# Kernel tuning notes

Measured on AMD Instinct MI355X. Metric: run time of the kernel, lower is better.

## Reference

```python
import jax, jax.numpy as jnp
import numpy as np

B, L1, L2, D, H, V, C = 32, 512, 16, 300, 300, 50000, 3


def setup_inputs() -> dict:
    key = jax.random.key(0)
    ks = jax.random.split(key, 20)
    s_emb = 1.0 / np.sqrt(D)
    s_h = 1.0 / np.sqrt(H)
    inp = {
        "context_ids": jax.random.randint(ks[0], (B, L1), 0, V),
        "aspect_ids": jax.random.randint(ks[1], (B, L2), 0, V),
        "context_masks": jnp.ones((B, L1), dtype=bool),
        "aspect_masks": jnp.ones((B, L2), dtype=bool),
        # frozen pretrained embedding table
        "emb": jax.random.normal(ks[2], (V, D), jnp.float32) * 0.1,
        # Attention module (no biases)
        "Wc": jax.random.normal(ks[3], (D, D), jnp.float32) * s_emb,
        "Wa": jax.random.normal(ks[4], (D, D), jnp.float32) * s_emb,
        "Vatt": jax.random.normal(ks[5], (1, D), jnp.float32) * s_emb,
        # self.W / self.V linears
        "Wlin": jax.random.normal(ks[6], (D, D), jnp.float32) * s_emb,
        "blin": jnp.zeros((D,), jnp.float32),
        "Vw": jax.random.normal(ks[7], (1, D), jnp.float32) * s_emb,
        "bVw": jnp.zeros((1,), jnp.float32),
        # bidirectional GRU, PyTorch layout: weight_ih (3H, D), weight_hh (3H, H)
        "wih_f": jax.random.normal(ks[8], (3 * H, D), jnp.float32) * s_h,
        "whh_f": jax.random.normal(ks[9], (3 * H, H), jnp.float32) * s_h,
        "bih_f": jnp.zeros((3 * H,), jnp.float32),
        "bhh_f": jnp.zeros((3 * H,), jnp.float32),
        "wih_b": jax.random.normal(ks[10], (3 * H, D), jnp.float32) * s_h,
        "whh_b": jax.random.normal(ks[11], (3 * H, H), jnp.float32) * s_h,
        "bih_b": jnp.zeros((3 * H,), jnp.float32),
        "bhh_b": jnp.zeros((3 * H,), jnp.float32),
        # output projection over concat(fwd, bwd) hidden
        "outW": jax.random.normal(ks[12], (C, 2 * H), jnp.float32) * (1.0 / np.sqrt(2 * H)),
        "outb": jnp.zeros((C,), jnp.float32),
    }
    return inp


def _gru_dir(x, wih, whh, bih, bhh, reverse):
    # x: (B, T, D) -> (B, T, H). PyTorch gate order: r, z, n.
    xg = jnp.einsum('btd,gd->btg', x, wih) + bih          # (B, T, 3H)
    xg = jnp.swapaxes(xg, 0, 1)                            # (T, B, 3H)

    def step(h, xg_t):
        rx, zx, nx = jnp.split(xg_t, 3, axis=-1)
        hg = h @ whh.T + bhh
        rh, zh, nh = jnp.split(hg, 3, axis=-1)
        r = jax.nn.sigmoid(rx + rh)
        z = jax.nn.sigmoid(zx + zh)
        n = jnp.tanh(nx + r * nh)
        h_new = (1.0 - z) * n + z * h
        return h_new, h_new

    h0 = jnp.zeros((x.shape[0], whh.shape[1]), x.dtype)
    _, hs = jax.lax.scan(step, h0, xg, reverse=reverse)
    return jnp.swapaxes(hs, 0, 1)                          # (B, T, H)


def reference(context_ids, aspect_ids, context_masks, aspect_masks, emb,
              Wc, Wa, Vatt, Wlin, blin, Vw, bVw,
              wih_f, whh_f, bih_f, bhh_f, wih_b, whh_b, bih_b, bhh_b,
              outW, outb):
    context = emb[context_ids]                             # (B, L1, D)
    aspect = emb[aspect_ids]                               # (B, L2, D)

    # additive (Bahdanau) attention: broadcast tanh score over (L1, L2)
    c = jnp.einsum('bld,ed->ble', context, Wc)             # (B, L1, D)
    a = jnp.einsum('bmd,ed->bme', aspect, Wa)              # (B, L2, D)
    s = jnp.tanh(c[:, :, None, :] + a[:, None, :, :])      # (B, L1, L2, D)
    scores = jnp.einsum('blmd,d->blm', s, Vatt[0])         # (B, L1, L2)
    alpha = jax.nn.softmax(scores, axis=-1)                # softmax over L2
    context_ = jnp.einsum('blm,bmd->bld', alpha, aspect)   # (B, L1, D)

    aaaa = jnp.tanh(jnp.einsum('bld,ed->ble', context, Wlin) + blin + context_)
    beta = jax.nn.softmax(jnp.einsum('bld,od->blo', aaaa, Vw) + bVw, axis=1)  # (B, L1, 1)

    h_f = _gru_dir(context, wih_f, whh_f, bih_f, bhh_f, reverse=False)
    h_b = _gru_dir(context, wih_b, whh_b, bih_b, bhh_b, reverse=True)
    senti_seq = jnp.concatenate([h_f, h_b], axis=-1)       # (B, L1, 2H)

    senti = jnp.einsum('bl,blh->bh', beta[..., 0], senti_seq)  # (B, 2H)
    logit = senti @ outW.T + outb                          # (B, C)
    return logit
```

## Files before the change

### kernel.cpp

```cpp
#include <hip/hip_runtime.h>

#define B_  32
#define L1_ 512
#define L2_ 16
#define D_  300
#define H_  300

__device__ __forceinline__ float sigmoid_fast(float x) {
    return 1.0f / (1.0f + __expf(-x));
}
__device__ __forceinline__ float tanh_fast(float x) {
    x = fminf(fmaxf(x, -15.0f), 15.0f);
    float e = __expf(2.0f * x);
    return (e - 1.0f) / (e + 1.0f);
}
__device__ __forceinline__ float sigmoid_acc(float x) {
    return 1.0f / (1.0f + expf(-x));
}
__device__ __forceinline__ float wred_sum(float v) {
    #pragma unroll
    for (int off = 32; off > 0; off >>= 1) v += __shfl_xor(v, off);
    return v;
}
__device__ __forceinline__ float wred_max(float v) {
    #pragma unroll
    for (int off = 32; off > 0; off >>= 1) v = fmaxf(v, __shfl_xor(v, off));
    return v;
}

__device__ __forceinline__ void store_pkt(long long* p, long long v) {
    asm volatile("global_store_dwordx2 %0, %1, off sc0 sc1" :: "v"(p), "v"(v) : "memory");
}
__device__ __forceinline__ long long load_pkt(const long long* p) {
    long long v;
    asm volatile("global_load_dwordx2 %0, %1, off sc0 sc1\n\t"
                 "s_waitcnt vmcnt(0)"
                 : "=v"(v) : "v"(p) : "memory");
    return v;
}

__global__ __launch_bounds__(256) void gather_kernel(const float* __restrict__ emb,
                                                     const int* __restrict__ ids,
                                                     float* __restrict__ out, int total) {
    for (int i = blockIdx.x * 256 + threadIdx.x; i < total; i += gridDim.x * 256) {
        int row = i / 75, c = i % 75;
        int id = ids[row];
        reinterpret_cast<float4*>(out)[i] =
            reinterpret_cast<const float4*>(emb + (size_t)id * 300)[c];
    }
}

#define TM 128
#define TN 64
#define TK 16
__global__ __launch_bounds__(256) void gemm_nt(const float* __restrict__ A,
                                               const float* __restrict__ W,
                                               const float* __restrict__ bias,
                                               float* __restrict__ C,
                                               int M, int N, int K) {
    __shared__ __align__(16) float As[TK][TM + 4];
    __shared__ __align__(16) float Bs[TK][TN + 4];
    const int tid = threadIdx.x;
    const int m0 = blockIdx.x * TM;
    const int n0 = blockIdx.y * TN;
    const int tx = tid & 15;
    const int ty = tid >> 4;
    const int lr = tid >> 2;
    const int lk = (tid & 3) << 2;

    float acc[8][4];
    #pragma unroll
    for (int i = 0; i < 8; ++i)
        #pragma unroll
        for (int j = 0; j < 4; ++j) acc[i][j] = 0.f;

    for (int k0 = 0; k0 < K; k0 += TK) {
        const bool kok = (k0 + lk + 3) < K;
        #pragma unroll
        for (int h = 0; h < 2; ++h) {
            float4 v = make_float4(0.f, 0.f, 0.f, 0.f);
            int m = m0 + lr + 64 * h;
            if (kok) v = *reinterpret_cast<const float4*>(&A[(size_t)m * K + k0 + lk]);
            As[lk + 0][lr + 64 * h] = v.x;
            As[lk + 1][lr + 64 * h] = v.y;
            As[lk + 2][lr + 64 * h] = v.z;
            As[lk + 3][lr + 64 * h] = v.w;
        }
        {
            float4 v = make_float4(0.f, 0.f, 0.f, 0.f);
            int n = n0 + lr;
            if (kok && n < N) v = *reinterpret_cast<const float4*>(&W[(size_t)n * K + k0 + lk]);
            Bs[lk + 0][lr] = v.x;
            Bs[lk + 1][lr] = v.y;
            Bs[lk + 2][lr] = v.z;
            Bs[lk + 3][lr] = v.w;
        }
        __syncthreads();
        #pragma unroll
        for (int k = 0; k < TK; ++k) {
            float4 a0 = *reinterpret_cast<const float4*>(&As[k][ty * 8]);
            float4 a1 = *reinterpret_cast<const float4*>(&As[k][ty * 8 + 4]);
            float4 bv = *reinterpret_cast<const float4*>(&Bs[k][tx * 4]);
            float av[8] = {a0.x, a0.y, a0.z, a0.w, a1.x, a1.y, a1.z, a1.w};
            float bb[4] = {bv.x, bv.y, bv.z, bv.w};
            #pragma unroll
            for (int i = 0; i < 8; ++i)
                #pragma unroll
                for (int j = 0; j < 4; ++j) acc[i][j] += av[i] * bb[j];
        }
        __syncthreads();
    }
    #pragma unroll
    for (int i = 0; i < 8; ++i) {
        int m = m0 + ty * 8 + i;
        #pragma unroll
        for (int j = 0; j < 4; ++j) {
            int n = n0 + tx * 4 + j;
            if (n < N) C[(size_t)m * N + n] = acc[i][j] + (bias ? bias[n] : 0.f);
        }
    }
}

__global__ __launch_bounds__(256) void attn_kernel(const float* __restrict__ c_proj,
                                                   const float* __restrict__ a_proj,
                                                   const float* __restrict__ asp_emb,
                                                   const float* __restrict__ lin,
                                                   const float* __restrict__ Vatt,
                                                   const float* __restrict__ Vw,
                                                   const float* __restrict__ bVw,
                                                   float* __restrict__ blogit) {
    const int b = blockIdx.y;
    const int chunk = blockIdx.x;
    __shared__ float sA[16 * 300];
    __shared__ float sE[16 * 300];
    __shared__ float sV[300];
    __shared__ float sW[300];
    const int tid = threadIdx.x;
    for (int i = tid; i < 16 * 300; i += 256) {
        sA[i] = a_proj[b * 4800 + i];
        sE[i] = asp_emb[b * 4800 + i];
    }
    for (int i = tid; i < 300; i += 256) {
        sV[i] = Vatt[i];
        sW[i] = Vw[i];
    }
    __syncthreads();
    const int wave = tid >> 6, lane = tid & 63;
    const float bvw = bVw[0];
    for (int li = 0; li < 4; ++li) {
        const int l = chunk * 16 + wave * 4 + li;
        const float* crow = c_proj + (size_t)(b * L1_ + l) * 300;
        float cr[5];
        #pragma unroll
        for (int i = 0; i < 5; ++i) {
            int d = lane + 64 * i;
            cr[i] = (d < 300) ? crow[d] : 0.f;
        }
        float sc[16];
        #pragma unroll
        for (int m = 0; m < 16; ++m) {
            float s = 0.f;
            #pragma unroll
            for (int i = 0; i < 5; ++i) {
                int d = lane + 64 * i;
                if (d < 300) s += tanh_fast(cr[i] + sA[m * 300 + d]) * sV[d];
            }
            s = wred_sum(s);
            sc[m] = s;
        }
        float mx = sc[0];
        #pragma unroll
        for (int m = 1; m < 16; ++m) mx = fmaxf(mx, sc[m]);
        float den = 0.f;
        #pragma unroll
        for (int m = 0; m < 16; ++m) {
            sc[m] = __expf(sc[m] - mx);
            den += sc[m];
        }
        const float inv = 1.f / den;
        const float* lrow = lin + (size_t)(b * L1_ + l) * 300;
        float acc = 0.f;
        #pragma unroll
        for (int i = 0; i < 5; ++i) {
            int d = lane + 64 * i;
            if (d < 300) {
                float cd = 0.f;
                #pragma unroll
                for (int m = 0; m < 16; ++m) cd += sc[m] * sE[m * 300 + d];
                acc += tanh_fast(lrow[d] + cd * inv) * sW[d];
            }
        }
        acc = wred_sum(acc);
        if (lane == 0) blogit[b * L1_ + l] = acc + bvw;
    }
}

__global__ __launch_bounds__(256) void beta_softmax_kernel(const float* __restrict__ x,
                                                           float* __restrict__ y) {
    const int b = blockIdx.x, tid = threadIdx.x;
    __shared__ float red[4];
    const int wave = tid >> 6, lane = tid & 63;
    float v0 = x[b * 512 + tid];
    float v1 = x[b * 512 + 256 + tid];
    float m = wred_max(fmaxf(v0, v1));
    if (lane == 0) red[wave] = m;
    __syncthreads();
    m = fmaxf(fmaxf(red[0], red[1]), fmaxf(red[2], red[3]));
    float e0 = __expf(v0 - m), e1 = __expf(v1 - m);
    float s = wred_sum(e0 + e1);
    __syncthreads();
    if (lane == 0) red[wave] = s;
    __syncthreads();
    s = red[0] + red[1] + red[2] + red[3];
    const float inv = 1.f / s;
    y[b * 512 + tid] = e0 * inv;
    y[b * 512 + 256 + tid] = e1 * inv;
}

__global__ __launch_bounds__(256, 1) void gru7_kernel(const float* __restrict__ xg_f,
                                                      const float* __restrict__ xg_b,
                                                      const float* __restrict__ whh_f,
                                                      const float* __restrict__ whh_b,
                                                      const float* __restrict__ bhh_f,
                                                      const float* __restrict__ bhh_b,
                                                      const float* __restrict__ beta,
                                                      long long* __restrict__ slot,
                                                      float* __restrict__ senti) {
    const int s = blockIdx.x;
    const int b = blockIdx.y;
    const int rev = blockIdx.z;
    const int g = rev * 32 + b;
    const float* xg  = rev ? xg_b : xg_f;
    const float* whh = rev ? whh_b : whh_f;
    const float* bhh = rev ? bhh_b : bhh_f;

    const int tid = threadIdx.x;
    const int e0 = s * 75;
    const bool act = tid < 225;
    const int gate = tid / 75;
    const int idx = tid % 75;

    __shared__ __align__(16) float hs[304];
    __shared__ float gg[3][80];

    float4 w4[75];
    float bh = 0.f;
    if (act) {
        const int row = gate * 300 + e0 + idx;
        bh = bhh[row];
        const float4* wp = reinterpret_cast<const float4*>(whh + (size_t)row * 300);
        #pragma unroll
        for (int j = 0; j < 75; ++j) w4[j] = wp[j];
    } else {
        #pragma unroll
        for (int j = 0; j < 75; ++j) w4[j] = make_float4(0.f, 0.f, 0.f, 0.f);
    }
    #pragma unroll
    for (int j = 0; j < 75; ++j)
        asm volatile("" : "+v"(w4[j].x), "+v"(w4[j].y), "+v"(w4[j].z), "+v"(w4[j].w));
    asm volatile("" : "+v"(bh));

    int fsl = 0, fli = 0;
    const long long* rp0 = nullptr;
    if (tid < 225) {
        fsl = tid / 75;
        if (fsl >= s) ++fsl;
        fli = tid % 75;
    }
    long long* wp0 = slot + ((size_t)g * 4 + s) * 80 + tid;
    const long long* rbase = slot + ((size_t)g * 4 + fsl) * 80 + fli;

    for (int i = tid; i < 304; i += 256) hs[i] = 0.f;
    float sacc = 0.f;
    int gaveup = 0;
    __syncthreads();

    const float4* hs4 = reinterpret_cast<const float4*>(hs);
    for (int step = 0; step < 512; ++step) {
        const int t = rev ? (511 - step) : step;
        float xr = 0.f, xz = 0.f, xn = 0.f, bt = 0.f;
        if (tid < 75) {
            const float* xrow = xg + (size_t)(b * 512 + t) * 900;
            const int e = e0 + tid;
            xr = xrow[e];
            xz = xrow[300 + e];
            xn = xrow[600 + e];
            bt = beta[b * 512 + t];
        }
        float a0 = 0.f, a1 = 0.f, a2 = 0.f, a3 = 0.f;
        #pragma unroll
        for (int j = 0; j < 72; j += 4) {
            float4 hv;
            hv = hs4[j];
            a0 = fmaf(w4[j].x, hv.x, a0); a0 = fmaf(w4[j].y, hv.y, a0);
            a0 = fmaf(w4[j].z, hv.z, a0); a0 = fmaf(w4[j].w, hv.w, a0);
            hv = hs4[j + 1];
            a1 = fmaf(w4[j + 1].x, hv.x, a1); a1 = fmaf(w4[j + 1].y, hv.y, a1);
            a1 = fmaf(w4[j + 1].z, hv.z, a1); a1 = fmaf(w4[j + 1].w, hv.w, a1);
            hv = hs4[j + 2];
            a2 = fmaf(w4[j + 2].x, hv.x, a2); a2 = fmaf(w4[j + 2].y, hv.y, a2);
            a2 = fmaf(w4[j + 2].z, hv.z, a2); a2 = fmaf(w4[j + 2].w, hv.w, a2);
            hv = hs4[j + 3];
            a3 = fmaf(w4[j + 3].x, hv.x, a3); a3 = fmaf(w4[j + 3].y, hv.y, a3);
            a3 = fmaf(w4[j + 3].z, hv.z, a3); a3 = fmaf(w4[j + 3].w, hv.w, a3);
        }
        {
            float4 hv;
            hv = hs4[72];
            a0 = fmaf(w4[72].x, hv.x, a0); a0 = fmaf(w4[72].y, hv.y, a0);
            a0 = fmaf(w4[72].z, hv.z, a0); a0 = fmaf(w4[72].w, hv.w, a0);
            hv = hs4[73];
            a1 = fmaf(w4[73].x, hv.x, a1); a1 = fmaf(w4[73].y, hv.y, a1);
            a1 = fmaf(w4[73].z, hv.z, a1); a1 = fmaf(w4[73].w, hv.w, a1);
            hv = hs4[74];
            a2 = fmaf(w4[74].x, hv.x, a2); a2 = fmaf(w4[74].y, hv.y, a2);
            a2 = fmaf(w4[74].z, hv.z, a2); a2 = fmaf(w4[74].w, hv.w, a2);
        }
        const float acc = bh + ((a0 + a1) + (a2 + a3));
        if (act) gg[gate][idx] = acc;
        __syncthreads();
        if (tid < 75) {
            const int e = e0 + tid;
            const float rr = sigmoid_acc(xr + gg[0][tid]);
            const float zz = sigmoid_acc(xz + gg[1][tid]);
            const float nn = tanhf(xn + rr * gg[2][tid]);
            const float hn = (1.f - zz) * nn + zz * hs[e];
            sacc = fmaf(bt, hn, sacc);
            hs[e] = hn;
            if (step < 511) {
                long long pkt = ((long long)(unsigned)step << 32) |
                                (unsigned)__float_as_int(hn);
                store_pkt(wp0 + (size_t)(step & 1) * 64 * 4 * 80, pkt);
            }
        }
        if (step == 511) break;
        if (tid < 225) {
            const long long* p = rbase + (size_t)(step & 1) * 64 * 4 * 80;
            long long v = 0;
            if (!gaveup) {
                int ok = 0;
                for (int it = 0; it < (1 << 16); ++it) {
                    v = load_pkt(p);
                    if (((int)(v >> 32)) == step) { ok = 1; break; }
                }
                if (!ok) gaveup = 1;
            } else {
                v = load_pkt(p);
            }
            hs[fsl * 75 + fli] = __int_as_float((int)(v & 0xffffffffLL));
        }
        __syncthreads();
    }
    if (tid < 75) senti[b * 600 + rev * 300 + e0 + tid] = sacc;
}

__global__ __launch_bounds__(64) void logits_kernel(const float* __restrict__ senti,
                                                    const float* __restrict__ outW,
                                                    const float* __restrict__ outb,
                                                    float* __restrict__ out) {
    const int b = blockIdx.x, lane = threadIdx.x;
    for (int c = 0; c < 3; ++c) {
        float s = 0.f;
        for (int hh = lane; hh < 600; hh += 64) s += senti[b * 600 + hh] * outW[c * 600 + hh];
        s = wred_sum(s);
        if (lane == 0) out[b * 3 + c] = s + outb[c];
    }
}

extern "C" void kernel_launch(void* const* d_in, const int* in_sizes, int n_in,
                              void* d_out, int out_size, void* d_ws, size_t ws_size,
                              hipStream_t stream) {
    const int* ctx_ids = (const int*)d_in[0];
    const int* asp_ids = (const int*)d_in[1];
    const float* emb   = (const float*)d_in[4];
    const float* Wc    = (const float*)d_in[5];
    const float* Wa    = (const float*)d_in[6];
    const float* Vatt  = (const float*)d_in[7];
    const float* Wlin  = (const float*)d_in[8];
    const float* blin  = (const float*)d_in[9];
    const float* Vw    = (const float*)d_in[10];
    const float* bVw   = (const float*)d_in[11];
    const float* wih_f = (const float*)d_in[12];
    const float* whh_f = (const float*)d_in[13];
    const float* bih_f = (const float*)d_in[14];
    const float* bhh_f = (const float*)d_in[15];
    const float* wih_b = (const float*)d_in[16];
    const float* whh_b = (const float*)d_in[17];
    const float* bih_b = (const float*)d_in[18];
    const float* bhh_b = (const float*)d_in[19];
    const float* outW  = (const float*)d_in[20];
    const float* outb  = (const float*)d_in[21];
    float* ws = (float*)d_ws;

    size_t o = 0;
    float* ctx_emb = ws + o; o += (size_t)B_ * L1_ * D_;
    float* asp_emb = ws + o; o += (size_t)B_ * L2_ * D_;
    float* c_proj  = ws + o; o += (size_t)B_ * L1_ * D_;
    float* a_proj  = ws + o; o += (size_t)B_ * L2_ * D_;
    float* lin_buf = ws + o; o += (size_t)B_ * L1_ * D_;
    float* xg_f    = ws + o; o += (size_t)B_ * L1_ * 3 * H_;
    float* xg_b    = ws + o; o += (size_t)B_ * L1_ * 3 * H_;
    float* blogit  = ws + o; o += (size_t)B_ * L1_;
    float* beta    = ws + o; o += (size_t)B_ * L1_;
    float* senti   = ws + o; o += (size_t)B_ * 2 * H_;
    o = (o + 1) & ~(size_t)1;
    long long* slot = (long long*)(ws + o);
    const size_t slot_ll = (size_t)2 * 64 * 4 * 80;
    o += slot_ll * 2;

    hipMemsetAsync(slot, 0xFF, slot_ll * sizeof(long long), stream);

    dim3 blk(256);
    const int tot_ctx = B_ * L1_ * 75;
    const int tot_asp = B_ * L2_ * 75;
    gather_kernel<<<dim3((tot_ctx + 255) / 256), blk, 0, stream>>>(emb, ctx_ids, ctx_emb, tot_ctx);
    gather_kernel<<<dim3((tot_asp + 255) / 256), blk, 0, stream>>>(emb, asp_ids, asp_emb, tot_asp);

    gemm_nt<<<dim3(16384 / 128, 5), blk, 0, stream>>>(ctx_emb, Wc, nullptr, c_proj, 16384, 300, 300);
    gemm_nt<<<dim3(16384 / 128, 5), blk, 0, stream>>>(ctx_emb, Wlin, blin, lin_buf, 16384, 300, 300);
    gemm_nt<<<dim3(512 / 128, 5), blk, 0, stream>>>(asp_emb, Wa, nullptr, a_proj, 512, 300, 300);
    gemm_nt<<<dim3(16384 / 128, 15), blk, 0, stream>>>(ctx_emb, wih_f, bih_f, xg_f, 16384, 900, 300);
    gemm_nt<<<dim3(16384 / 128, 15), blk, 0, stream>>>(ctx_emb, wih_b, bih_b, xg_b, 16384, 900, 300);

    attn_kernel<<<dim3(32, 32), blk, 0, stream>>>(c_proj, a_proj, asp_emb, lin_buf, Vatt, Vw, bVw, blogit);
    beta_softmax_kernel<<<dim3(32), blk, 0, stream>>>(blogit, beta);
    gru7_kernel<<<dim3(4, 32, 2), blk, 0, stream>>>(xg_f, xg_b, whh_f, whh_b, bhh_f, bhh_b,
                                                    beta, slot, senti);
    logits_kernel<<<dim3(32), dim3(64), 0, stream>>>(senti, outW, outb, (float*)d_out);
}
```

Before: 2.372 ms.

## Split GRU producer and poller waves, batch packet loads, pad GEMM B tile

In the GRU recurrence, the 75 threads that compute and publish the new hidden slice now sit in a different wave from the threads that poll for the other slices. The pollers are now threads 128-255, each fetching two packets per poll with an s_sleep backoff, so publishing and polling overlap instead of running one after the other in the same waves. The final step is handled separately so it skips the exchange. The GEMM B tile in shared memory gets padded columns to reduce bank conflicts on the float4 reads. The sleep could add latency to each of the 512 serial steps.

```diff
diff --git a/kernel.cpp b/kernel.cpp
--- a/kernel.cpp
+++ b/kernel.cpp
@@ -37,6 +37,13 @@
                  "s_waitcnt vmcnt(0)"
                  : "=v"(v) : "v"(p) : "memory");
     return v;
+}
+__device__ __forceinline__ void load_pkt2(const long long* p1, const long long* p2,
+                                          long long& v1, long long& v2) {
+    asm volatile("global_load_dwordx2 %0, %2, off sc0 sc1\n\t"
+                 "global_load_dwordx2 %1, %3, off sc0 sc1\n\t"
+                 "s_waitcnt vmcnt(0)"
+                 : "=&v"(v1), "=v"(v2) : "v"(p1), "v"(p2) : "memory");
 }
 
 __global__ __launch_bounds__(256) void gather_kernel(const float* __restrict__ emb,
@@ -53,13 +60,14 @@
 #define TM 128
 #define TN 64
 #define TK 16
+__device__ __forceinline__ int bcol(int c) { return c + ((c >> 5) << 2); }
 __global__ __launch_bounds__(256) void gemm_nt(const float* __restrict__ A,
                                                const float* __restrict__ W,
                                                const float* __restrict__ bias,
                                                float* __restrict__ C,
                                                int M, int N, int K) {
     __shared__ __align__(16) float As[TK][TM + 4];
-    __shared__ __align__(16) float Bs[TK][TN + 4];
+    __shared__ __align__(16) float Bs[TK][76];
     const int tid = threadIdx.x;
     const int m0 = blockIdx.x * TM;
     const int n0 = blockIdx.y * TN;
@@ -90,17 +98,18 @@
             float4 v = make_float4(0.f, 0.f, 0.f, 0.f);
             int n = n0 + lr;
             if (kok && n < N) v = *reinterpret_cast<const float4*>(&W[(size_t)n * K + k0 + lk]);
-            Bs[lk + 0][lr] = v.x;
-            Bs[lk + 1][lr] = v.y;
-            Bs[lk + 2][lr] = v.z;
-            Bs[lk + 3][lr] = v.w;
+            const int lrp = bcol(lr);
+            Bs[lk + 0][lrp] = v.x;
+            Bs[lk + 1][lrp] = v.y;
+            Bs[lk + 2][lrp] = v.z;
+            Bs[lk + 3][lrp] = v.w;
         }
         __syncthreads();
         #pragma unroll
         for (int k = 0; k < TK; ++k) {
             float4 a0 = *reinterpret_cast<const float4*>(&As[k][ty * 8]);
             float4 a1 = *reinterpret_cast<const float4*>(&As[k][ty * 8 + 4]);
-            float4 bv = *reinterpret_cast<const float4*>(&Bs[k][tx * 4]);
+            float4 bv = *reinterpret_cast<const float4*>(&Bs[k][bcol(tx * 4)]);
             float av[8] = {a0.x, a0.y, a0.z, a0.w, a1.x, a1.y, a1.z, a1.w};
             float bb[4] = {bv.x, bv.y, bv.z, bv.w};
             #pragma unroll
@@ -217,7 +226,7 @@
     y[b * 512 + 256 + tid] = e1 * inv;
 }
 
-__global__ __launch_bounds__(256, 1) void gru7_kernel(const float* __restrict__ xg_f,
+__global__ __launch_bounds__(256, 1) void gru8_kernel(const float* __restrict__ xg_f,
                                                       const float* __restrict__ xg_b,
                                                       const float* __restrict__ whh_f,
                                                       const float* __restrict__ whh_b,
@@ -260,15 +269,24 @@
         asm volatile("" : "+v"(w4[j].x), "+v"(w4[j].y), "+v"(w4[j].z), "+v"(w4[j].w));
     asm volatile("" : "+v"(bh));
 
-    int fsl = 0, fli = 0;
-    const long long* rp0 = nullptr;
-    if (tid < 225) {
-        fsl = tid / 75;
-        if (fsl >= s) ++fsl;
-        fli = tid % 75;
+    int fsl1 = 0, fli1 = 0, fsl2 = 0, fli2 = 0;
+    bool has2 = false;
+    if (tid >= 128) {
+        const int i1 = tid - 128;
+        fsl1 = i1 / 75; if (fsl1 >= s) ++fsl1;
+        fli1 = i1 % 75;
+        const int i2 = i1 + 128;
+        if (i2 < 225) {
+            has2 = true;
+            fsl2 = i2 / 75; if (fsl2 >= s) ++fsl2;
+            fli2 = i2 % 75;
+        } else {
+            fsl2 = fsl1; fli2 = fli1;
+        }
     }
     long long* wp0 = slot + ((size_t)g * 4 + s) * 80 + tid;
-    const long long* rbase = slot + ((size_t)g * 4 + fsl) * 80 + fli;
+    const long long* rb1 = slot + ((size_t)g * 4 + fsl1) * 80 + fli1;
+    const long long* rb2 = slot + ((size_t)g * 4 + fsl2) * 80 + fli2;
 
     for (int i = tid; i < 304; i += 256) hs[i] = 0.f;
     float sacc = 0.f;
@@ -319,6 +337,16 @@
         const float acc = bh + ((a0 + a1) + (a2 + a3));
         if (act) gg[gate][idx] = acc;
         __syncthreads();
+        if (step == 511) {
+            if (tid < 75) {
+                const float rr = sigmoid_acc(xr + gg[0][tid]);
+                const float zz = sigmoid_acc(xz + gg[1][tid]);
+                const float nn = tanhf(xn + rr * gg[2][tid]);
+                const float hn = (1.f - zz) * nn + zz * hs[e0 + tid];
+                sacc = fmaf(bt, hn, sacc);
+            }
+            break;
+        }
         if (tid < 75) {
             const int e = e0 + tid;
             const float rr = sigmoid_acc(xr + gg[0][tid]);
@@ -327,27 +355,27 @@
             const float hn = (1.f - zz) * nn + zz * hs[e];
             sacc = fmaf(bt, hn, sacc);
             hs[e] = hn;
-            if (step < 511) {
-                long long pkt = ((long long)(unsigned)step << 32) |
-                                (unsigned)__float_as_int(hn);
-                store_pkt(wp0 + (size_t)(step & 1) * 64 * 4 * 80, pkt);
+            long long pkt = ((long long)(unsigned)step << 32) |
+                            (unsigned)__float_as_int(hn);
+            store_pkt(wp0 + (size_t)(step & 1) * 64 * 4 * 80, pkt);
+        } else if (tid >= 128) {
+            const size_t po = (size_t)(step & 1) * 64 * 4 * 80;
+            const long long* p1 = rb1 + po;
+            const long long* p2 = rb2 + po;
+            long long v1 = 0, v2 = 0;
+            if (!gaveup) {
+                load_pkt2(p1, p2, v1, v2);
+                int it = 0;
+                while (((int)(v1 >> 32)) != step || ((int)(v2 >> 32)) != step) {
+                    if (++it >= (1 << 16)) { gaveup = 1; break; }
+                    __builtin_amdgcn_s_sleep(1);
+                    load_pkt2(p1, p2, v1, v2);
+                }
+            } else {
+                load_pkt2(p1, p2, v1, v2);
             }
-        }
-        if (step == 511) break;
-        if (tid < 225) {
-            const long long* p = rbase + (size_t)(step & 1) * 64 * 4 * 80;
-            long long v = 0;
-            if (!gaveup) {
-                int ok = 0;
-                for (int it = 0; it < (1 << 16); ++it) {
-                    v = load_pkt(p);
-                    if (((int)(v >> 32)) == step) { ok = 1; break; }
-                }
-                if (!ok) gaveup = 1;
-            } else {
-                v = load_pkt(p);
-            }
-            hs[fsl * 75 + fli] = __int_as_float((int)(v & 0xffffffffLL));
+            hs[fsl1 * 75 + fli1] = __int_as_float((int)(v1 & 0xffffffffLL));
+            if (has2) hs[fsl2 * 75 + fli2] = __int_as_float((int)(v2 & 0xffffffffLL));
         }
         __syncthreads();
     }
@@ -424,7 +452,7 @@
 
     attn_kernel<<<dim3(32, 32), blk, 0, stream>>>(c_proj, a_proj, asp_emb, lin_buf, Vatt, Vw, bVw, blogit);
     beta_softmax_kernel<<<dim3(32), blk, 0, stream>>>(blogit, beta);
-    gru7_kernel<<<dim3(4, 32, 2), blk, 0, stream>>>(xg_f, xg_b, whh_f, whh_b, bhh_f, bhh_b,
+    gru8_kernel<<<dim3(4, 32, 2), blk, 0, stream>>>(xg_f, xg_b, whh_f, whh_b, bhh_f, bhh_b,
                                                     beta, slot, senti);
     logits_kernel<<<dim3(32), dim3(64), 0, stream>>>(senti, outW, outb, (float*)d_out);
 }
```

Measured after the change: 2.464 ms. 1.04x slower.
